# Kernel optimization log

Hardware: AMD Instinct MI355X
Metric: run time of the kernel (lower is better)

The kernel has to match this reference:

```python
import math
import jax, jax.numpy as jnp
import numpy as np

E = 1024
H = 16
HD = E // H
MLP = 4 * E
EPS = 1e-6


def setup_inputs() -> dict:
    key = jax.random.key(0)
    ks = jax.random.split(key, 12)
    s = lambda fan_in: 1.0 / math.sqrt(fan_in)
    return {
        "x": jax.random.normal(ks[0], (8, 1024, E), dtype=jnp.float32),
        "ln1_g": jnp.ones((E,), jnp.float32),
        "ln1_b": jnp.zeros((E,), jnp.float32),
        "w_qkv": jax.random.normal(ks[1], (E, 3 * E), jnp.float32) * s(E),
        "b_qkv": jnp.zeros((3 * E,), jnp.float32),
        "w_o": jax.random.normal(ks[2], (E, E), jnp.float32) * s(E),
        "b_o": jnp.zeros((E,), jnp.float32),
        "ln2_g": jnp.ones((E,), jnp.float32),
        "ln2_b": jnp.zeros((E,), jnp.float32),
        "w_fc1": jax.random.normal(ks[3], (E, MLP), jnp.float32) * s(E),
        "b_fc1": jnp.zeros((MLP,), jnp.float32),
        "w_fc2": jax.random.normal(ks[4], (MLP, E), jnp.float32) * s(MLP),
        "b_fc2": jnp.zeros((E,), jnp.float32),
    }


def _layernorm(x, g, b):
    mu = jnp.mean(x, axis=-1, keepdims=True)
    var = jnp.mean(jnp.square(x - mu), axis=-1, keepdims=True)
    return (x - mu) * jax.lax.rsqrt(var + EPS) * g + b


def _attn(x, w_qkv, b_qkv, w_o, b_o):
    B, N, _ = x.shape
    qkv = (x @ w_qkv + b_qkv).reshape(B, N, 3, H, HD)
    q, k, v = qkv[:, :, 0], qkv[:, :, 1], qkv[:, :, 2]  # [B,N,H,HD]
    scores = jnp.einsum("bnhd,bmhd->bhnm", q, k) / math.sqrt(HD)
    probs = jax.nn.softmax(scores, axis=-1)
    out = jnp.einsum("bhnm,bmhd->bnhd", probs, v).reshape(B, N, H * HD)
    return out @ w_o + b_o


def reference(x, ln1_g, ln1_b, w_qkv, b_qkv, w_o, b_o, ln2_g, ln2_b,
              w_fc1, b_fc1, w_fc2, b_fc2):
    # pre-LN attention block with residual
    x = x + _attn(_layernorm(x, ln1_g, ln1_b), w_qkv, b_qkv, w_o, b_o)
    # pre-LN MLP block with residual (exact GELU, matching torch nn.GELU)
    h = _layernorm(x, ln2_g, ln2_b) @ w_fc1 + b_fc1
    h = jax.nn.gelu(h, approximate=False)
    x = x + (h @ w_fc2 + b_fc2)
    return x
```

## Files before the change

kernel.cpp:

```cpp
#include <hip/hip_runtime.h>
#include <stdint.h>

typedef unsigned short u16;
typedef __bf16 bf16x8 __attribute__((ext_vector_type(8)));
typedef float f32x4 __attribute__((ext_vector_type(4)));

#define GLD16(gp, lp) __builtin_amdgcn_global_load_lds( \
    (__attribute__((address_space(1))) void*)(uintptr_t)(gp), \
    (__attribute__((address_space(3))) void*)(uintptr_t)(lp), 16, 0, 0)

__device__ __forceinline__ u16 f2bf(float f) {
  uint32_t u = __builtin_bit_cast(uint32_t, f);
  u += 0x7FFFu + ((u >> 16) & 1u);
  return (u16)(u >> 16);
}

__global__ __launch_bounds__(256) void wtrans(const float* __restrict__ w,
                                              u16* __restrict__ wt, int K, int Nn) {
  __shared__ float tile[64][68];
  const int c0 = blockIdx.x << 6, r0 = blockIdx.y << 6;
  const int t = threadIdx.x, tr = t >> 2, tc = t & 3;
#pragma unroll
  for (int p = 0; p < 4; ++p) {
    float4 v = *(const float4*)&w[(size_t)(r0 + tr) * Nn + c0 + tc * 4 + p * 16];
    tile[tr][tc * 4 + p * 16 + 0] = v.x;
    tile[tr][tc * 4 + p * 16 + 1] = v.y;
    tile[tr][tc * 4 + p * 16 + 2] = v.z;
    tile[tr][tc * 4 + p * 16 + 3] = v.w;
  }
  __syncthreads();
#pragma unroll
  for (int p = 0; p < 4; ++p) {
    u16 e0 = f2bf(tile[tc * 4 + p * 16 + 0][tr]);
    u16 e1 = f2bf(tile[tc * 4 + p * 16 + 1][tr]);
    u16 e2 = f2bf(tile[tc * 4 + p * 16 + 2][tr]);
    u16 e3 = f2bf(tile[tc * 4 + p * 16 + 3][tr]);
    uint2 o;
    o.x = (uint32_t)e0 | ((uint32_t)e1 << 16);
    o.y = (uint32_t)e2 | ((uint32_t)e3 << 16);
    *(uint2*)&wt[(size_t)(c0 + tr) * K + r0 + tc * 4 + p * 16] = o;
  }
}

__global__ __launch_bounds__(256) void lnorm(const float* x, const float* __restrict__ g,
                                             const float* __restrict__ bta,
                                             u16* __restrict__ out) {
  const int lane = threadIdx.x & 63, wid = threadIdx.x >> 6;
  const size_t token = (size_t)blockIdx.x * 4 + wid;
  const float* row = x + token * 1024;
  float v[16];
#pragma unroll
  for (int i = 0; i < 4; ++i) {
    float4 f = *(const float4*)&row[(lane + i * 64) * 4];
    v[i * 4 + 0] = f.x; v[i * 4 + 1] = f.y; v[i * 4 + 2] = f.z; v[i * 4 + 3] = f.w;
  }
  float s = 0.f, s2 = 0.f;
#pragma unroll
  for (int i = 0; i < 16; ++i) { s += v[i]; s2 += v[i] * v[i]; }
  for (int off = 1; off < 64; off <<= 1) {
    s += __shfl_xor(s, off);
    s2 += __shfl_xor(s2, off);
  }
  const float mu = s * (1.0f / 1024.0f);
  const float var = s2 * (1.0f / 1024.0f) - mu * mu;
  const float rstd = rsqrtf(var + 1e-6f);
  u16* orow = out + token * 1024;
#pragma unroll
  for (int i = 0; i < 4; ++i) {
    const int c = (lane + i * 64) * 4;
    float4 gv = *(const float4*)&g[c];
    float4 bv = *(const float4*)&bta[c];
    u16 e0 = f2bf((v[i * 4 + 0] - mu) * rstd * gv.x + bv.x);
    u16 e1 = f2bf((v[i * 4 + 1] - mu) * rstd * gv.y + bv.y);
    u16 e2 = f2bf((v[i * 4 + 2] - mu) * rstd * gv.z + bv.z);
    u16 e3 = f2bf((v[i * 4 + 3] - mu) * rstd * gv.w + bv.w);
    uint2 o;
    o.x = (uint32_t)e0 | ((uint32_t)e1 << 16);
    o.y = (uint32_t)e2 | ((uint32_t)e3 << 16);
    *(uint2*)&orow[c] = o;
  }
}

template <int EPI>
__global__ __launch_bounds__(256) void gemm128(const u16* __restrict__ A,
                                               const u16* __restrict__ Bt,
                                               const float* __restrict__ bias,
                                               const float* res, void* Cout,
                                               int Ndim, int K, float qscale, int qlimit) {
  __shared__ __align__(16) u16 ldsA[2][4096];
  __shared__ __align__(16) u16 ldsB[2][4096];
  const int tid = threadIdx.x;
  const int lane = tid & 63;
  const int wid = tid >> 6;
  const int wm = wid & 1, wn = wid >> 1;
  const int m0 = blockIdx.y << 7, n0 = blockIdx.x << 7;

  const int srow = lane >> 2;
  const int slc = (lane & 3) ^ ((srow ^ (srow >> 2)) & 3);
  const u16* Ag = A + (size_t)(m0 + 32 * wid + srow) * K + slc * 8;
  const u16* Bg = Bt + (size_t)(n0 + 32 * wid + srow) * K + slc * 8;
  const size_t rstep = (size_t)16 * K;

  const int rrow = lane & 15;
  const int rc = ((lane >> 4) ^ ((rrow ^ (rrow >> 2)) & 3)) * 16;

  const f32x4 fzero = {0.f, 0.f, 0.f, 0.f};
  f32x4 acc[4][4];
#pragma unroll
  for (int i = 0; i < 4; ++i)
#pragma unroll
    for (int j = 0; j < 4; ++j) acc[i][j] = fzero;

  const int nk = K >> 5;
  GLD16(Ag, &ldsA[0][(2 * wid + 0) * 512]);
  GLD16(Ag + rstep, &ldsA[0][(2 * wid + 1) * 512]);
  GLD16(Bg, &ldsB[0][(2 * wid + 0) * 512]);
  GLD16(Bg + rstep, &ldsB[0][(2 * wid + 1) * 512]);
  __syncthreads();
  for (int kt = 0; kt < nk; ++kt) {
    const int cur = kt & 1;
    if (kt + 1 < nk) {
      const u16* a = Ag + (size_t)(kt + 1) * 32;
      const u16* b = Bg + (size_t)(kt + 1) * 32;
      GLD16(a, &ldsA[cur ^ 1][(2 * wid + 0) * 512]);
      GLD16(a + rstep, &ldsA[cur ^ 1][(2 * wid + 1) * 512]);
      GLD16(b, &ldsB[cur ^ 1][(2 * wid + 0) * 512]);
      GLD16(b + rstep, &ldsB[cur ^ 1][(2 * wid + 1) * 512]);
    }
    bf16x8 af[4], bfr[4];
#pragma unroll
    for (int mf = 0; mf < 4; ++mf)
      af[mf] = *(const bf16x8*)((const char*)&ldsA[cur][0] +
                                (wm * 64 + mf * 16 + rrow) * 64 + rc);
#pragma unroll
    for (int nf = 0; nf < 4; ++nf)
      bfr[nf] = *(const bf16x8*)((const char*)&ldsB[cur][0] +
                                 (wn * 64 + nf * 16 + rrow) * 64 + rc);
#pragma unroll
    for (int mf = 0; mf < 4; ++mf)
#pragma unroll
      for (int nf = 0; nf < 4; ++nf)
        acc[mf][nf] =
            __builtin_amdgcn_mfma_f32_16x16x32_bf16(af[mf], bfr[nf], acc[mf][nf], 0, 0, 0);
    __syncthreads();
  }
  const int g4 = (lane >> 4) << 2;
  const float cs = (EPI == 0 && n0 < qlimit) ? qscale : 1.0f;
#pragma unroll
  for (int nf = 0; nf < 4; ++nf) {
    const int col = n0 + wn * 64 + nf * 16 + rrow;
    const float bv = bias[col];
#pragma unroll
    for (int mf = 0; mf < 4; ++mf) {
#pragma unroll
      for (int r = 0; r < 4; ++r) {
        const int row = m0 + wm * 64 + mf * 16 + g4 + r;
        float v = acc[mf][nf][r] + bv;
        if (EPI == 0) v *= cs;
        if (EPI == 1) v = 0.5f * v * (1.0f + erff(v * 0.70710678118654752f));
        if (EPI == 2) {
          v += res[(size_t)row * Ndim + col];
          ((float*)Cout)[(size_t)row * Ndim + col] = v;
        } else {
          ((u16*)Cout)[(size_t)row * Ndim + col] = f2bf(v);
        }
      }
    }
  }
}

__global__ __launch_bounds__(256) void vtrans(const u16* __restrict__ qkv,
                                              u16* __restrict__ vt) {
  const int bh = blockIdx.y, b = bh >> 4, h = bh & 15;
  const int n0 = blockIdx.x << 6;
  __shared__ __align__(16) u16 tile[64][72];
  const int t = threadIdx.x, r = t >> 2, c = t & 3;
  const u16* src = qkv + (size_t)((b << 10) + n0 + r) * 3072 + 2048 + (h << 6);
#pragma unroll
  for (int p = 0; p < 2; ++p)
    *(uint4*)&tile[r][(c * 2 + p) * 8] = *(const uint4*)(src + (c * 2 + p) * 8);
  __syncthreads();
  u16* dst = vt + (size_t)((bh << 6) + r) * 1024 + n0;
#pragma unroll
  for (int p = 0; p < 2; ++p) {
    u16 o[8];
#pragma unroll
    for (int j = 0; j < 8; ++j) o[j] = tile[(c * 2 + p) * 8 + j][r];
    uint4 w;
    w.x = (uint32_t)o[0] | ((uint32_t)o[1] << 16);
    w.y = (uint32_t)o[2] | ((uint32_t)o[3] << 16);
    w.z = (uint32_t)o[4] | ((uint32_t)o[5] << 16);
    w.w = (uint32_t)o[6] | ((uint32_t)o[7] << 16);
    *(uint4*)&dst[(c * 2 + p) * 8] = w;
  }
}

__global__ __launch_bounds__(256) void attn64(const u16* __restrict__ qkv,
                                              const u16* __restrict__ vt,
                                              u16* __restrict__ aout) {
  const int bh = blockIdx.y, b = bh >> 4, h = bh & 15;
  const int q0 = blockIdx.x << 6;
  const int tid = threadIdx.x, lane = tid & 63, wid = tid >> 6;
  __shared__ __align__(16) u16 kl[4096];
  __shared__ __align__(16) u16 vl[4096];
  __shared__ __align__(16) u16 pl[4][1152];

  const int rrow = lane & 15;
  const int g = lane >> 4;
  const u16* qrow = qkv + (size_t)((b << 10) + q0 + (wid << 4) + rrow) * 3072 + (h << 6);
  bf16x8 qf0 = *(const bf16x8*)(qrow + (g << 3));
  bf16x8 qf1 = *(const bf16x8*)(qrow + 32 + (g << 3));

  const int sr = lane >> 3;
  const int lc = (lane & 7) ^ sr;
  const u16* kbase = qkv + (size_t)(b << 10) * 3072 + 1024 + (h << 6) +
                     (size_t)(16 * wid + sr) * 3072 + lc * 8;
  const u16* vbase = vt + (size_t)(bh << 6) * 1024 + (size_t)(16 * wid + sr) * 1024 + lc * 8;

  const f32x4 fzero = {0.f, 0.f, 0.f, 0.f};
  f32x4 oacc[4];
#pragma unroll
  for (int i = 0; i < 4; ++i) oacc[i] = fzero;
  f32x4 lacc = fzero;
  const int rcb = lane & 7;
  u16* plw = &pl[wid][0];

  for (int t = 0; t < 16; ++t) {
    const int kt0 = t << 6;
    GLD16(kbase + (size_t)kt0 * 3072, &kl[(2 * wid + 0) * 512]);
    GLD16(kbase + (size_t)kt0 * 3072 + 8 * 3072, &kl[(2 * wid + 1) * 512]);
    GLD16(vbase + kt0, &vl[(2 * wid + 0) * 512]);
    GLD16(vbase + kt0 + 8 * 1024, &vl[(2 * wid + 1) * 512]);
    __syncthreads();

    f32x4 s4[4];
#pragma unroll
    for (int i = 0; i < 4; ++i) s4[i] = fzero;
#pragma unroll
    for (int nf = 0; nf < 4; ++nf) {
      bf16x8 k0 = *(const bf16x8*)((const char*)kl + (nf * 16 + rrow) * 128 +
                                   ((g + 0) ^ rcb) * 16);
      bf16x8 k1 = *(const bf16x8*)((const char*)kl + (nf * 16 + rrow) * 128 +
                                   ((g + 4) ^ rcb) * 16);
      s4[nf] = __builtin_amdgcn_mfma_f32_16x16x32_bf16(k0, qf0, s4[nf], 0, 0, 0);
      s4[nf] = __builtin_amdgcn_mfma_f32_16x16x32_bf16(k1, qf1, s4[nf], 0, 0, 0);
    }

#pragma unroll
    for (int nf = 0; nf < 4; ++nf) {
      float p0 = exp2f(s4[nf][0]);
      float p1 = exp2f(s4[nf][1]);
      float p2 = exp2f(s4[nf][2]);
      float p3 = exp2f(s4[nf][3]);
      f32x4 pv = {p0, p1, p2, p3};
      lacc += pv;
      uint32_t a0 = __builtin_bit_cast(uint32_t, p0) + 0x8000u;
      uint32_t a1 = __builtin_bit_cast(uint32_t, p1) + 0x8000u;
      uint32_t a2 = __builtin_bit_cast(uint32_t, p2) + 0x8000u;
      uint32_t a3 = __builtin_bit_cast(uint32_t, p3) + 0x8000u;
      uint2 w;
      w.x = __builtin_amdgcn_perm(a1, a0, 0x07060302);
      w.y = __builtin_amdgcn_perm(a3, a2, 0x07060302);
      *(uint2*)(plw + rrow * 72 + nf * 16 + (g << 2)) = w;
    }

    bf16x8 pf0 = *(const bf16x8*)((const char*)plw + rrow * 144 + (g << 4));
    bf16x8 pf1 = *(const bf16x8*)((const char*)plw + rrow * 144 + (g << 4) + 64);
#pragma unroll
    for (int nf = 0; nf < 4; ++nf) {
      bf16x8 v0 = *(const bf16x8*)((const char*)vl + (nf * 16 + rrow) * 128 +
                                   ((g + 0) ^ rcb) * 16);
      bf16x8 v1 = *(const bf16x8*)((const char*)vl + (nf * 16 + rrow) * 128 +
                                   ((g + 4) ^ rcb) * 16);
      oacc[nf] = __builtin_amdgcn_mfma_f32_16x16x32_bf16(pf0, v0, oacc[nf], 0, 0, 0);
      oacc[nf] = __builtin_amdgcn_mfma_f32_16x16x32_bf16(pf1, v1, oacc[nf], 0, 0, 0);
    }
    __syncthreads();
  }

  float lsum = lacc[0] + lacc[1] + lacc[2] + lacc[3];
  lsum += __shfl_xor(lsum, 16);
  lsum += __shfl_xor(lsum, 32);
  const float inv = 1.0f / lsum;
  float invq[4];
#pragma unroll
  for (int r = 0; r < 4; ++r) {
    int bi = __builtin_amdgcn_ds_bpermute(((g << 2) + r) << 2,
                                          __builtin_bit_cast(int, inv));
    invq[r] = __builtin_bit_cast(float, bi);
  }
  u16* ob = aout + (size_t)((b << 10) + q0 + (wid << 4)) * 1024 + (h << 6);
#pragma unroll
  for (int nf = 0; nf < 4; ++nf)
#pragma unroll
    for (int r = 0; r < 4; ++r)
      ob[(size_t)(g * 4 + r) * 1024 + nf * 16 + rrow] = f2bf(oacc[nf][r] * invq[r]);
}

extern "C" void kernel_launch(void* const* d_in, const int* in_sizes, int n_in,
                              void* d_out, int out_size, void* d_ws, size_t ws_size,
                              hipStream_t stream) {
  const float* x = (const float*)d_in[0];
  const float* ln1_g = (const float*)d_in[1];
  const float* ln1_b = (const float*)d_in[2];
  const float* w_qkv = (const float*)d_in[3];
  const float* b_qkv = (const float*)d_in[4];
  const float* w_o = (const float*)d_in[5];
  const float* b_o = (const float*)d_in[6];
  const float* ln2_g = (const float*)d_in[7];
  const float* ln2_b = (const float*)d_in[8];
  const float* w_fc1 = (const float*)d_in[9];
  const float* b_fc1 = (const float*)d_in[10];
  const float* w_fc2 = (const float*)d_in[11];
  const float* b_fc2 = (const float*)d_in[12];
  float* out = (float*)d_out;

  char* w = (char*)d_ws;
  u16* wqkvT = (u16*)w; w += (size_t)3072 * 1024 * 2;
  u16* woT   = (u16*)w; w += (size_t)1024 * 1024 * 2;
  u16* wfc1T = (u16*)w; w += (size_t)4096 * 1024 * 2;
  u16* wfc2T = (u16*)w; w += (size_t)1024 * 4096 * 2;
  u16* xn    = (u16*)w; w += (size_t)8192 * 1024 * 2;
  u16* qkvb  = (u16*)w; w += (size_t)8192 * 3072 * 2;
  u16* vtb   = (u16*)w; w += (size_t)128 * 64 * 1024 * 2;
  u16* attnb = (u16*)w; w += (size_t)8192 * 1024 * 2;
  u16* hbuf  = qkvb;

  const float QS = 0.18033688011112042f;

  wtrans<<<dim3(48, 16), 256, 0, stream>>>(w_qkv, wqkvT, 1024, 3072);
  wtrans<<<dim3(16, 16), 256, 0, stream>>>(w_o, woT, 1024, 1024);
  wtrans<<<dim3(64, 16), 256, 0, stream>>>(w_fc1, wfc1T, 1024, 4096);
  wtrans<<<dim3(16, 64), 256, 0, stream>>>(w_fc2, wfc2T, 4096, 1024);

  lnorm<<<2048, 256, 0, stream>>>(x, ln1_g, ln1_b, xn);
  gemm128<0><<<dim3(24, 64), 256, 0, stream>>>(xn, wqkvT, b_qkv, nullptr, qkvb, 3072, 1024, QS, 1024);
  vtrans<<<dim3(16, 128), 256, 0, stream>>>(qkvb, vtb);
  attn64<<<dim3(16, 128), 256, 0, stream>>>(qkvb, vtb, attnb);
  gemm128<2><<<dim3(8, 64), 256, 0, stream>>>(attnb, woT, b_o, x, out, 1024, 1024, 1.f, 0);
  lnorm<<<2048, 256, 0, stream>>>(out, ln2_g, ln2_b, xn);
  gemm128<1><<<dim3(32, 64), 256, 0, stream>>>(xn, wfc1T, b_fc1, nullptr, hbuf, 4096, 1024, 1.f, 0);
  gemm128<2><<<dim3(8, 64), 256, 0, stream>>>(hbuf, wfc2T, b_fc2, out, out, 1024, 4096, 1.f, 0);
}
```

Baseline: 434.9 us.

## Replace 128x128 GEMM with 256-row tiles, triple-buffered pipeline and XCD swizzle

Replaces the 128x128 four-wave GEMM with an eight-wave kernel using 256xBN tiles (BN 256 for the QKV/FC1 GEMMs, 128 for the output projections). It adds a three-stage LDS pipeline with explicit vmcnt waits and a single barrier per k-step, and interleaves prefetch issues with MFMA groups under s_setprio. Block indices are remapped so consecutive blocks on the same XCD share M rows. The goal is more data reuse per tile, fewer barriers and better L2 locality, at the cost of more LDS and registers per block and fewer blocks in the grid.

Result: faster. 418.8 us (-3.7%).

```diff
diff --git a/kernel.cpp b/kernel.cpp
--- a/kernel.cpp
+++ b/kernel.cpp
@@ -8,6 +8,9 @@
 #define GLD16(gp, lp) __builtin_amdgcn_global_load_lds( \
     (__attribute__((address_space(1))) void*)(uintptr_t)(gp), \
     (__attribute__((address_space(3))) void*)(uintptr_t)(lp), 16, 0, 0)
+
+#define WAITVM(N) asm volatile("s_waitcnt vmcnt(" #N ")" ::: "memory")
+#define BARRIER() asm volatile("s_barrier" ::: "memory")
 
 __device__ __forceinline__ u16 f2bf(float f) {
   uint32_t u = __builtin_bit_cast(uint32_t, f);
@@ -81,82 +84,141 @@
   }
 }
 
-template <int EPI>
-__global__ __launch_bounds__(256) void gemm128(const u16* __restrict__ A,
-                                               const u16* __restrict__ Bt,
-                                               const float* __restrict__ bias,
-                                               const float* res, void* Cout,
-                                               int Ndim, int K, float qscale, int qlimit) {
-  __shared__ __align__(16) u16 ldsA[2][4096];
-  __shared__ __align__(16) u16 ldsB[2][4096];
-  const int tid = threadIdx.x;
-  const int lane = tid & 63;
-  const int wid = tid >> 6;
-  const int wm = wid & 1, wn = wid >> 1;
-  const int m0 = blockIdx.y << 7, n0 = blockIdx.x << 7;
-
-  const int srow = lane >> 2;
-  const int slc = (lane & 3) ^ ((srow ^ (srow >> 2)) & 3);
-  const u16* Ag = A + (size_t)(m0 + 32 * wid + srow) * K + slc * 8;
-  const u16* Bg = Bt + (size_t)(n0 + 32 * wid + srow) * K + slc * 8;
-  const size_t rstep = (size_t)16 * K;
+template <int EPI, int BN>
+__global__ __launch_bounds__(512, 2) void gemm256(const u16* __restrict__ A,
+                                                  const u16* __restrict__ Bt,
+                                                  const float* __restrict__ bias,
+                                                  const float* res, void* Cout,
+                                                  int Ndim, int K, float qscale,
+                                                  int qlimit, int gn) {
+  constexpr int MF = (BN == 256) ? 8 : 4;
+  constexpr int HMF = MF / 2;
+  constexpr int WMS = (BN == 256) ? 128 : 64;
+  constexpr int SLOT = 8192 + BN * 32;
+  __shared__ __align__(16) u16 lds[3][SLOT];
+
+  const int tid = threadIdx.x, lane = tid & 63, wid = tid >> 6;
+  const int wm = (BN == 256) ? (wid >> 2) : (wid >> 1);
+  const int wn = (BN == 256) ? (wid & 3) : (wid & 1);
+
+  const int wg = blockIdx.x;
+  const int swz = (wg & 7) * ((int)gridDim.x >> 3) + (wg >> 3);
+  const int mblk = swz / gn;
+  const int nb = swz - mblk * gn;
+  const int m0 = mblk << 8;
+  const int n0 = nb * BN;
+
+  const int srow = tid >> 2;
+  const int slc = (tid & 3) ^ ((srow ^ (srow >> 2)) & 3);
+  const u16* Ag = A + (size_t)(m0 + srow) * K + slc * 8;
+  const u16* Bg = Bt + (size_t)(n0 + srow) * K + slc * 8;
+  const size_t rstep = (size_t)128 * K;
 
   const int rrow = lane & 15;
   const int rc = ((lane >> 4) ^ ((rrow ^ (rrow >> 2)) & 3)) * 16;
+  const int aRow0 = wm * WMS + rrow;
+  const int bRow0 = wn * 64 + rrow;
 
   const f32x4 fzero = {0.f, 0.f, 0.f, 0.f};
-  f32x4 acc[4][4];
-#pragma unroll
-  for (int i = 0; i < 4; ++i)
+  f32x4 acc[MF][4];
+#pragma unroll
+  for (int i = 0; i < MF; ++i)
 #pragma unroll
     for (int j = 0; j < 4; ++j) acc[i][j] = fzero;
 
   const int nk = K >> 5;
-  GLD16(Ag, &ldsA[0][(2 * wid + 0) * 512]);
-  GLD16(Ag + rstep, &ldsA[0][(2 * wid + 1) * 512]);
-  GLD16(Bg, &ldsB[0][(2 * wid + 0) * 512]);
-  GLD16(Bg + rstep, &ldsB[0][(2 * wid + 1) * 512]);
-  __syncthreads();
+
+#define SA0(kt, s) GLD16(Ag + (size_t)(kt) * 32, &lds[s][wid * 512])
+#define SA1(kt, s) GLD16(Ag + rstep + (size_t)(kt) * 32, &lds[s][4096 + wid * 512])
+#define SB0(kt, s) GLD16(Bg + (size_t)(kt) * 32, &lds[s][8192 + wid * 512])
+#define SB1(kt, s) GLD16(Bg + rstep + (size_t)(kt) * 32, &lds[s][12288 + wid * 512])
+
+  SA0(0, 0); SA1(0, 0); SB0(0, 0);
+  if constexpr (BN == 256) SB1(0, 0);
+  SA0(1, 1); SA1(1, 1); SB0(1, 1);
+  if constexpr (BN == 256) SB1(1, 1);
+
+  int cs = 0, ss = 2;
   for (int kt = 0; kt < nk; ++kt) {
-    const int cur = kt & 1;
     if (kt + 1 < nk) {
-      const u16* a = Ag + (size_t)(kt + 1) * 32;
-      const u16* b = Bg + (size_t)(kt + 1) * 32;
-      GLD16(a, &ldsA[cur ^ 1][(2 * wid + 0) * 512]);
-      GLD16(a + rstep, &ldsA[cur ^ 1][(2 * wid + 1) * 512]);
-      GLD16(b, &ldsB[cur ^ 1][(2 * wid + 0) * 512]);
-      GLD16(b + rstep, &ldsB[cur ^ 1][(2 * wid + 1) * 512]);
-    }
-    bf16x8 af[4], bfr[4];
-#pragma unroll
-    for (int mf = 0; mf < 4; ++mf)
-      af[mf] = *(const bf16x8*)((const char*)&ldsA[cur][0] +
-                                (wm * 64 + mf * 16 + rrow) * 64 + rc);
-#pragma unroll
-    for (int nf = 0; nf < 4; ++nf)
-      bfr[nf] = *(const bf16x8*)((const char*)&ldsB[cur][0] +
-                                 (wn * 64 + nf * 16 + rrow) * 64 + rc);
-#pragma unroll
-    for (int mf = 0; mf < 4; ++mf)
-#pragma unroll
-      for (int nf = 0; nf < 4; ++nf)
-        acc[mf][nf] =
-            __builtin_amdgcn_mfma_f32_16x16x32_bf16(af[mf], bfr[nf], acc[mf][nf], 0, 0, 0);
-    __syncthreads();
-  }
+      if constexpr (BN == 256) WAITVM(4); else WAITVM(3);
+    } else {
+      WAITVM(0);
+    }
+    BARRIER();
+    const bool pf = (kt + 2 < nk);
+    const char* la = (const char*)&lds[cs][0];
+    const char* lb = la + 16384;
+    bf16x8 af[MF], bv[4];
+    if (pf) SA0(kt + 2, ss);
+#pragma unroll
+    for (int i = 0; i < HMF; ++i)
+      af[i] = *(const bf16x8*)(la + (aRow0 + i * 16) * 64 + rc);
+    bv[0] = *(const bf16x8*)(lb + (bRow0 + 0) * 64 + rc);
+    bv[1] = *(const bf16x8*)(lb + (bRow0 + 16) * 64 + rc);
+    __builtin_amdgcn_s_setprio(1);
+#pragma unroll
+    for (int i = 0; i < HMF; ++i)
+#pragma unroll
+      for (int j = 0; j < 2; ++j)
+        acc[i][j] = __builtin_amdgcn_mfma_f32_16x16x32_bf16(af[i], bv[j], acc[i][j], 0, 0, 0);
+    __builtin_amdgcn_s_setprio(0);
+    if (pf) SA1(kt + 2, ss);
+#pragma unroll
+    for (int i = 0; i < HMF; ++i)
+      af[HMF + i] = *(const bf16x8*)(la + (aRow0 + (HMF + i) * 16) * 64 + rc);
+    __builtin_amdgcn_s_setprio(1);
+#pragma unroll
+    for (int i = 0; i < HMF; ++i)
+#pragma unroll
+      for (int j = 0; j < 2; ++j)
+        acc[HMF + i][j] =
+            __builtin_amdgcn_mfma_f32_16x16x32_bf16(af[HMF + i], bv[j], acc[HMF + i][j], 0, 0, 0);
+    __builtin_amdgcn_s_setprio(0);
+    if (pf) SB0(kt + 2, ss);
+    bv[2] = *(const bf16x8*)(lb + (bRow0 + 32) * 64 + rc);
+    bv[3] = *(const bf16x8*)(lb + (bRow0 + 48) * 64 + rc);
+    __builtin_amdgcn_s_setprio(1);
+#pragma unroll
+    for (int i = 0; i < HMF; ++i)
+#pragma unroll
+      for (int j = 0; j < 2; ++j)
+        acc[HMF + i][2 + j] =
+            __builtin_amdgcn_mfma_f32_16x16x32_bf16(af[HMF + i], bv[2 + j], acc[HMF + i][2 + j], 0, 0, 0);
+    __builtin_amdgcn_s_setprio(0);
+    if constexpr (BN == 256) {
+      if (pf) SB1(kt + 2, ss);
+    }
+    __builtin_amdgcn_s_setprio(1);
+#pragma unroll
+    for (int i = 0; i < HMF; ++i)
+#pragma unroll
+      for (int j = 0; j < 2; ++j)
+        acc[i][2 + j] =
+            __builtin_amdgcn_mfma_f32_16x16x32_bf16(af[i], bv[2 + j], acc[i][2 + j], 0, 0, 0);
+    __builtin_amdgcn_s_setprio(0);
+
+    cs = (cs == 2) ? 0 : cs + 1;
+    ss = (ss == 2) ? 0 : ss + 1;
+  }
+#undef SA0
+#undef SA1
+#undef SB0
+#undef SB1
+
   const int g4 = (lane >> 4) << 2;
-  const float cs = (EPI == 0 && n0 < qlimit) ? qscale : 1.0f;
 #pragma unroll
   for (int nf = 0; nf < 4; ++nf) {
     const int col = n0 + wn * 64 + nf * 16 + rrow;
-    const float bv = bias[col];
-#pragma unroll
-    for (int mf = 0; mf < 4; ++mf) {
+    const float bvb = bias[col];
+    const float csf = (EPI == 0 && col < qlimit) ? qscale : 1.0f;
+#pragma unroll
+    for (int mf = 0; mf < MF; ++mf) {
 #pragma unroll
       for (int r = 0; r < 4; ++r) {
-        const int row = m0 + wm * 64 + mf * 16 + g4 + r;
-        float v = acc[mf][nf][r] + bv;
-        if (EPI == 0) v *= cs;
+        const int row = m0 + wm * WMS + mf * 16 + g4 + r;
+        float v = acc[mf][nf][r] + bvb;
+        if (EPI == 0) v *= csf;
         if (EPI == 1) v = 0.5f * v * (1.0f + erff(v * 0.70710678118654752f));
         if (EPI == 2) {
           v += res[(size_t)row * Ndim + col];
@@ -334,11 +396,11 @@
   wtrans<<<dim3(16, 64), 256, 0, stream>>>(w_fc2, wfc2T, 4096, 1024);
 
   lnorm<<<2048, 256, 0, stream>>>(x, ln1_g, ln1_b, xn);
-  gemm128<0><<<dim3(24, 64), 256, 0, stream>>>(xn, wqkvT, b_qkv, nullptr, qkvb, 3072, 1024, QS, 1024);
+  gemm256<0, 256><<<384, 512, 0, stream>>>(xn, wqkvT, b_qkv, nullptr, qkvb, 3072, 1024, QS, 1024, 12);
   vtrans<<<dim3(16, 128), 256, 0, stream>>>(qkvb, vtb);
   attn64<<<dim3(16, 128), 256, 0, stream>>>(qkvb, vtb, attnb);
-  gemm128<2><<<dim3(8, 64), 256, 0, stream>>>(attnb, woT, b_o, x, out, 1024, 1024, 1.f, 0);
+  gemm256<2, 128><<<256, 512, 0, stream>>>(attnb, woT, b_o, x, out, 1024, 1024, 1.f, 0, 8);
   lnorm<<<2048, 256, 0, stream>>>(out, ln2_g, ln2_b, xn);
-  gemm128<1><<<dim3(32, 64), 256, 0, stream>>>(xn, wfc1T, b_fc1, nullptr, hbuf, 4096, 1024, 1.f, 0);
-  gemm128<2><<<dim3(8, 64), 256, 0, stream>>>(hbuf, wfc2T, b_fc2, out, out, 1024, 4096, 1.f, 0);
-}
+  gemm256<1, 256><<<512, 512, 0, stream>>>(xn, wfc1T, b_fc1, nullptr, hbuf, 4096, 1024, 1.f, 0, 16);
+  gemm256<2, 128><<<256, 512, 0, stream>>>(hbuf, wfc2T, b_fc2, out, out, 1024, 4096, 1.f, 0, 8);
+}
```

## Replace GEMM with 256x128 tile, 4-stage LDS pipeline and XCD-aware block swizzle

Applied to the files above, without the earlier changes.

Rewrites the bf16 MFMA GEMM to use 512-thread blocks computing 256x128 tiles. Global-to-LDS loads now run through a 4-stage ring with explicit vmcnt waits and raw barriers, and MFMA issue priority is raised around the compute phases. A 1D grid is remapped with a swizzle so neighbouring tiles land on the same XCD for L2 reuse. The goal is to hide global memory latency and raise MFMA utilisation, at the cost of 96KB of LDS per block and fragile hand-managed wait counts.

Result: faster. 416.3 us (-4.3%).

```diff
diff --git a/kernel.cpp b/kernel.cpp
--- a/kernel.cpp
+++ b/kernel.cpp
@@ -8,6 +8,10 @@
 #define GLD16(gp, lp) __builtin_amdgcn_global_load_lds( \
     (__attribute__((address_space(1))) void*)(uintptr_t)(gp), \
     (__attribute__((address_space(3))) void*)(uintptr_t)(lp), 16, 0, 0)
+
+#define WAITVM(N) asm volatile("s_waitcnt vmcnt(" #N ")" ::: "memory")
+#define BARRIER() asm volatile("s_barrier" ::: "memory")
+#define MM(a, b, c) __builtin_amdgcn_mfma_f32_16x16x32_bf16(a, b, c, 0, 0, 0)
 
 __device__ __forceinline__ u16 f2bf(float f) {
   uint32_t u = __builtin_bit_cast(uint32_t, f);
@@ -82,27 +86,39 @@
 }
 
 template <int EPI>
-__global__ __launch_bounds__(256) void gemm128(const u16* __restrict__ A,
-                                               const u16* __restrict__ Bt,
-                                               const float* __restrict__ bias,
-                                               const float* res, void* Cout,
-                                               int Ndim, int K, float qscale, int qlimit) {
-  __shared__ __align__(16) u16 ldsA[2][4096];
-  __shared__ __align__(16) u16 ldsB[2][4096];
-  const int tid = threadIdx.x;
-  const int lane = tid & 63;
-  const int wid = tid >> 6;
-  const int wm = wid & 1, wn = wid >> 1;
-  const int m0 = blockIdx.y << 7, n0 = blockIdx.x << 7;
-
-  const int srow = lane >> 2;
-  const int slc = (lane & 3) ^ ((srow ^ (srow >> 2)) & 3);
-  const u16* Ag = A + (size_t)(m0 + 32 * wid + srow) * K + slc * 8;
-  const u16* Bg = Bt + (size_t)(n0 + 32 * wid + srow) * K + slc * 8;
-  const size_t rstep = (size_t)16 * K;
-
-  const int rrow = lane & 15;
-  const int rc = ((lane >> 4) ^ ((rrow ^ (rrow >> 2)) & 3)) * 16;
+__global__ __launch_bounds__(512, 2) void gemmp(const u16* __restrict__ A,
+                                                const u16* __restrict__ Bt,
+                                                const float* __restrict__ bias,
+                                                const float* res, void* Cout,
+                                                int Ndim, int K, float qscale,
+                                                int qlimit, int gn) {
+  __shared__ __align__(16) u16 lds[4][12288];
+  const int tid = threadIdx.x, lane = tid & 63, wid = tid >> 6;
+  const int wm = wid >> 1, wn = wid & 1;
+
+  const int wg = blockIdx.x;
+  const int swz = (wg & 7) * ((int)gridDim.x >> 3) + (wg >> 3);
+  const int mblk = swz / gn, nb = swz - mblk * gn;
+  const int m0 = mblk << 8, n0 = nb << 7;
+
+  const int srow = tid >> 2;
+  const int sc = (tid & 3) ^ ((tid >> 3) & 3);
+  const u16* Ag0 = A + (size_t)(m0 + srow) * K + sc * 8;
+  const u16* Ag1 = Ag0 + (size_t)128 * K;
+  const u16* Bg = Bt + (size_t)(n0 + srow) * K + sc * 8;
+
+  u16* lb = &lds[0][0];
+  const int rrow = lane & 15, g = lane >> 4;
+  const int xg = g ^ ((rrow >> 1) & 3);
+  const int aoff = (wm * 64 + rrow) * 64 + xg * 16;
+  const int boff = 16384 + (wn * 64 + rrow) * 64 + xg * 16;
+  const char* pA[4];
+  const char* pB[4];
+#pragma unroll
+  for (int s = 0; s < 4; ++s) {
+    pA[s] = (const char*)lb + s * 24576 + aoff;
+    pB[s] = (const char*)lb + s * 24576 + boff;
+  }
 
   const f32x4 fzero = {0.f, 0.f, 0.f, 0.f};
   f32x4 acc[4][4];
@@ -111,52 +127,81 @@
 #pragma unroll
     for (int j = 0; j < 4; ++j) acc[i][j] = fzero;
 
-  const int nk = K >> 5;
-  GLD16(Ag, &ldsA[0][(2 * wid + 0) * 512]);
-  GLD16(Ag + rstep, &ldsA[0][(2 * wid + 1) * 512]);
-  GLD16(Bg, &ldsB[0][(2 * wid + 0) * 512]);
-  GLD16(Bg + rstep, &ldsB[0][(2 * wid + 1) * 512]);
-  __syncthreads();
-  for (int kt = 0; kt < nk; ++kt) {
-    const int cur = kt & 1;
-    if (kt + 1 < nk) {
-      const u16* a = Ag + (size_t)(kt + 1) * 32;
-      const u16* b = Bg + (size_t)(kt + 1) * 32;
-      GLD16(a, &ldsA[cur ^ 1][(2 * wid + 0) * 512]);
-      GLD16(a + rstep, &ldsA[cur ^ 1][(2 * wid + 1) * 512]);
-      GLD16(b, &ldsB[cur ^ 1][(2 * wid + 0) * 512]);
-      GLD16(b + rstep, &ldsB[cur ^ 1][(2 * wid + 1) * 512]);
-    }
-    bf16x8 af[4], bfr[4];
-#pragma unroll
-    for (int mf = 0; mf < 4; ++mf)
-      af[mf] = *(const bf16x8*)((const char*)&ldsA[cur][0] +
-                                (wm * 64 + mf * 16 + rrow) * 64 + rc);
-#pragma unroll
-    for (int nf = 0; nf < 4; ++nf)
-      bfr[nf] = *(const bf16x8*)((const char*)&ldsB[cur][0] +
-                                 (wn * 64 + nf * 16 + rrow) * 64 + rc);
-#pragma unroll
-    for (int mf = 0; mf < 4; ++mf)
-#pragma unroll
-      for (int nf = 0; nf < 4; ++nf)
-        acc[mf][nf] =
-            __builtin_amdgcn_mfma_f32_16x16x32_bf16(af[mf], bfr[nf], acc[mf][nf], 0, 0, 0);
-    __syncthreads();
-  }
+#define STG(tt, ss) do { \
+    GLD16(Ag0 + (tt) * 32, lb + (ss) * 12288 + wid * 512); \
+    GLD16(Ag1 + (tt) * 32, lb + (ss) * 12288 + 4096 + wid * 512); \
+    GLD16(Bg + (tt) * 32, lb + (ss) * 12288 + 8192 + wid * 512); \
+  } while (0)
+
+#define PH(dt, DOSTG, WVA) do { \
+    bf16x8 af0 = *(const bf16x8*)(pA[(dt)] + 0); \
+    bf16x8 af1 = *(const bf16x8*)(pA[(dt)] + 1024); \
+    bf16x8 af2 = *(const bf16x8*)(pA[(dt)] + 2048); \
+    bf16x8 af3 = *(const bf16x8*)(pA[(dt)] + 3072); \
+    bf16x8 bf0 = *(const bf16x8*)(pB[(dt)] + 0); \
+    bf16x8 bf1 = *(const bf16x8*)(pB[(dt)] + 1024); \
+    bf16x8 bf2 = *(const bf16x8*)(pB[(dt)] + 2048); \
+    bf16x8 bf3 = *(const bf16x8*)(pB[(dt)] + 3072); \
+    if (DOSTG) STG((dt) + 3, ((dt) + 3) & 3); \
+    WVA; \
+    BARRIER(); \
+    __builtin_amdgcn_s_setprio(1); \
+    acc[0][0] = MM(af0, bf0, acc[0][0]); \
+    acc[1][0] = MM(af1, bf0, acc[1][0]); \
+    acc[2][0] = MM(af2, bf0, acc[2][0]); \
+    acc[3][0] = MM(af3, bf0, acc[3][0]); \
+    acc[0][1] = MM(af0, bf1, acc[0][1]); \
+    acc[1][1] = MM(af1, bf1, acc[1][1]); \
+    acc[2][1] = MM(af2, bf1, acc[2][1]); \
+    acc[3][1] = MM(af3, bf1, acc[3][1]); \
+    acc[0][2] = MM(af0, bf2, acc[0][2]); \
+    acc[1][2] = MM(af1, bf2, acc[1][2]); \
+    acc[2][2] = MM(af2, bf2, acc[2][2]); \
+    acc[3][2] = MM(af3, bf2, acc[3][2]); \
+    acc[0][3] = MM(af0, bf3, acc[0][3]); \
+    acc[1][3] = MM(af1, bf3, acc[1][3]); \
+    acc[2][3] = MM(af2, bf3, acc[2][3]); \
+    acc[3][3] = MM(af3, bf3, acc[3][3]); \
+    __builtin_amdgcn_s_setprio(0); \
+    BARRIER(); \
+  } while (0)
+
+  const int nT = K >> 5;
+  STG(0, 0);
+  STG(1, 1);
+  STG(2, 2);
+  WAITVM(6);
+  BARRIER();
+  const int nG = nT >> 2;
+  for (int gi = 0; gi < nG - 1; ++gi) {
+    PH(0, true, WAITVM(6));
+    PH(1, true, WAITVM(6));
+    PH(2, true, WAITVM(6));
+    PH(3, true, WAITVM(6));
+    Ag0 += 128;
+    Ag1 += 128;
+    Bg += 128;
+  }
+  PH(0, true, WAITVM(6));
+  PH(1, false, WAITVM(3));
+  PH(2, false, WAITVM(0));
+  PH(3, false, (void)0);
+#undef PH
+#undef STG
+
   const int g4 = (lane >> 4) << 2;
-  const float cs = (EPI == 0 && n0 < qlimit) ? qscale : 1.0f;
 #pragma unroll
   for (int nf = 0; nf < 4; ++nf) {
     const int col = n0 + wn * 64 + nf * 16 + rrow;
-    const float bv = bias[col];
+    const float bvb = bias[col];
+    const float csf = (EPI == 0 && col < qlimit) ? qscale : 1.0f;
 #pragma unroll
     for (int mf = 0; mf < 4; ++mf) {
 #pragma unroll
       for (int r = 0; r < 4; ++r) {
         const int row = m0 + wm * 64 + mf * 16 + g4 + r;
-        float v = acc[mf][nf][r] + bv;
-        if (EPI == 0) v *= cs;
+        float v = acc[mf][nf][r] + bvb;
+        if (EPI == 0) v *= csf;
         if (EPI == 1) v = 0.5f * v * (1.0f + erff(v * 0.70710678118654752f));
         if (EPI == 2) {
           v += res[(size_t)row * Ndim + col];
@@ -334,11 +379,11 @@
   wtrans<<<dim3(16, 64), 256, 0, stream>>>(w_fc2, wfc2T, 4096, 1024);
 
   lnorm<<<2048, 256, 0, stream>>>(x, ln1_g, ln1_b, xn);
-  gemm128<0><<<dim3(24, 64), 256, 0, stream>>>(xn, wqkvT, b_qkv, nullptr, qkvb, 3072, 1024, QS, 1024);
+  gemmp<0><<<768, 512, 0, stream>>>(xn, wqkvT, b_qkv, nullptr, qkvb, 3072, 1024, QS, 1024, 24);
   vtrans<<<dim3(16, 128), 256, 0, stream>>>(qkvb, vtb);
   attn64<<<dim3(16, 128), 256, 0, stream>>>(qkvb, vtb, attnb);
-  gemm128<2><<<dim3(8, 64), 256, 0, stream>>>(attnb, woT, b_o, x, out, 1024, 1024, 1.f, 0);
+  gemmp<2><<<256, 512, 0, stream>>>(attnb, woT, b_o, x, out, 1024, 1024, 1.f, 0, 8);
   lnorm<<<2048, 256, 0, stream>>>(out, ln2_g, ln2_b, xn);
-  gemm128<1><<<dim3(32, 64), 256, 0, stream>>>(xn, wfc1T, b_fc1, nullptr, hbuf, 4096, 1024, 1.f, 0);
-  gemm128<2><<<dim3(8, 64), 256, 0, stream>>>(hbuf, wfc2T, b_fc2, out, out, 1024, 4096, 1.f, 0);
-}
+  gemmp<1><<<1024, 512, 0, stream>>>(xn, wfc1T, b_fc1, nullptr, hbuf, 4096, 1024, 1.f, 0, 32);
+  gemmp<2><<<256, 512, 0, stream>>>(hbuf, wfc2T, b_fc2, out, out, 1024, 4096, 1.f, 0, 8);
+}
```

## Replace 128x128 GEMM with 256x256 tiles, 4-stage pipeline, split-K atomics

Applied to the files above, without the earlier changes.

Replaces the 128x128 double-buffered GEMM with a 512-thread 256x256 tile kernel. It uses a 4-slot LDS ring with two tiles in flight, explicit vmcnt waits and raw barriers, MFMA priority raising, and a grouped workgroup swizzle for L2 reuse. The residual GEMMs (w_o, fc2) now use split-K=2 with atomicAdd into an output that a device memcpy of x pre-initialises. The aim is more data reuse per tile, deeper latency hiding and better occupancy of the small-N GEMMs. The cost is larger register and LDS pressure, atomic traffic, nondeterministic summation order and an extra 32MB copy.

Result: slower. 480.5 us (+10.5%).

```diff
diff --git a/kernel.cpp b/kernel.cpp
--- a/kernel.cpp
+++ b/kernel.cpp
@@ -8,6 +8,10 @@
 #define GLD16(gp, lp) __builtin_amdgcn_global_load_lds( \
     (__attribute__((address_space(1))) void*)(uintptr_t)(gp), \
     (__attribute__((address_space(3))) void*)(uintptr_t)(lp), 16, 0, 0)
+
+#define WAITVM(N) asm volatile("s_waitcnt vmcnt(" #N ")" ::: "memory")
+#define BARRIER() asm volatile("s_barrier" ::: "memory")
+#define MM(a, b, c) __builtin_amdgcn_mfma_f32_16x16x32_bf16(a, b, c, 0, 0, 0)
 
 __device__ __forceinline__ u16 f2bf(float f) {
   uint32_t u = __builtin_bit_cast(uint32_t, f);
@@ -82,85 +86,92 @@
 }
 
 template <int EPI>
-__global__ __launch_bounds__(256) void gemm128(const u16* __restrict__ A,
-                                               const u16* __restrict__ Bt,
-                                               const float* __restrict__ bias,
-                                               const float* res, void* Cout,
-                                               int Ndim, int K, float qscale, int qlimit) {
-  __shared__ __align__(16) u16 ldsA[2][4096];
-  __shared__ __align__(16) u16 ldsB[2][4096];
-  const int tid = threadIdx.x;
-  const int lane = tid & 63;
-  const int wid = tid >> 6;
-  const int wm = wid & 1, wn = wid >> 1;
-  const int m0 = blockIdx.y << 7, n0 = blockIdx.x << 7;
-
-  const int srow = lane >> 2;
-  const int slc = (lane & 3) ^ ((srow ^ (srow >> 2)) & 3);
-  const u16* Ag = A + (size_t)(m0 + 32 * wid + srow) * K + slc * 8;
-  const u16* Bg = Bt + (size_t)(n0 + 32 * wid + srow) * K + slc * 8;
-  const size_t rstep = (size_t)16 * K;
-
-  const int rrow = lane & 15;
-  const int rc = ((lane >> 4) ^ ((rrow ^ (rrow >> 2)) & 3)) * 16;
+__global__ __launch_bounds__(512, 2) void gemmk(const u16* __restrict__ A,
+                                                const u16* __restrict__ Bt,
+                                                const float* __restrict__ bias,
+                                                void* Cout, int Ndim, int K, int nT,
+                                                float qscale, int qlimit, int gn) {
+  __shared__ __align__(16) u16 lds[4][16384];
+  const int tid = threadIdx.x, lane = tid & 63, wid = tid >> 6;
+  const int wm = wid >> 2, wn = wid & 3;
+
+  const int wg = blockIdx.x;
+  const int swz = (wg & 7) * ((int)gridDim.x >> 3) + (wg >> 3);
+  const int mblk = swz / gn, nb = swz - mblk * gn;
+  const int m0 = mblk << 8, n0 = nb << 8;
+  const int koff = blockIdx.y * (nT << 5);
+
+  const int srow = tid >> 2;
+  const int gsub = (tid & 3) ^ ((tid >> 3) & 3);
+  const u16* Ag = A + koff + (size_t)(m0 + srow) * K + gsub * 8;
+  const u16* Bg = Bt + koff + (size_t)(n0 + srow) * K + gsub * 8;
+  const size_t rstep = (size_t)128 * K;
+  char* lb = (char*)&lds[0][0];
+
+  const int rrow = lane & 15, g = lane >> 4;
+  const int xg = g ^ ((rrow >> 1) & 3);
+  const int aoff = (wm * 128 + rrow) * 64 + xg * 16;
+  const int boff = 16384 + (wn * 64 + rrow) * 64 + xg * 16;
 
   const f32x4 fzero = {0.f, 0.f, 0.f, 0.f};
-  f32x4 acc[4][4];
-#pragma unroll
-  for (int i = 0; i < 4; ++i)
+  f32x4 acc[8][4];
+#pragma unroll
+  for (int i = 0; i < 8; ++i)
 #pragma unroll
     for (int j = 0; j < 4; ++j) acc[i][j] = fzero;
 
-  const int nk = K >> 5;
-  GLD16(Ag, &ldsA[0][(2 * wid + 0) * 512]);
-  GLD16(Ag + rstep, &ldsA[0][(2 * wid + 1) * 512]);
-  GLD16(Bg, &ldsB[0][(2 * wid + 0) * 512]);
-  GLD16(Bg + rstep, &ldsB[0][(2 * wid + 1) * 512]);
-  __syncthreads();
-  for (int kt = 0; kt < nk; ++kt) {
-    const int cur = kt & 1;
-    if (kt + 1 < nk) {
-      const u16* a = Ag + (size_t)(kt + 1) * 32;
-      const u16* b = Bg + (size_t)(kt + 1) * 32;
-      GLD16(a, &ldsA[cur ^ 1][(2 * wid + 0) * 512]);
-      GLD16(a + rstep, &ldsA[cur ^ 1][(2 * wid + 1) * 512]);
-      GLD16(b, &ldsB[cur ^ 1][(2 * wid + 0) * 512]);
-      GLD16(b + rstep, &ldsB[cur ^ 1][(2 * wid + 1) * 512]);
-    }
-    bf16x8 af[4], bfr[4];
-#pragma unroll
-    for (int mf = 0; mf < 4; ++mf)
-      af[mf] = *(const bf16x8*)((const char*)&ldsA[cur][0] +
-                                (wm * 64 + mf * 16 + rrow) * 64 + rc);
+#define STG(tt) do { \
+    char* d_ = lb + ((tt) & 3) * 32768; \
+    GLD16(Ag + (size_t)(tt) * 32, d_ + tid * 16); \
+    GLD16(Ag + rstep + (size_t)(tt) * 32, d_ + 8192 + tid * 16); \
+    GLD16(Bg + (size_t)(tt) * 32, d_ + 16384 + tid * 16); \
+    GLD16(Bg + rstep + (size_t)(tt) * 32, d_ + 24576 + tid * 16); \
+  } while (0)
+
+  STG(0);
+  STG(1);
+  WAITVM(4);
+  BARRIER();
+  for (int t = 0; t < nT; ++t) {
+    if (t + 2 < nT) STG(t + 2);
+    const char* sb = lb + (t & 3) * 32768;
+    bf16x8 bfr[4], af[8];
 #pragma unroll
     for (int nf = 0; nf < 4; ++nf)
-      bfr[nf] = *(const bf16x8*)((const char*)&ldsB[cur][0] +
-                                 (wn * 64 + nf * 16 + rrow) * 64 + rc);
-#pragma unroll
-    for (int mf = 0; mf < 4; ++mf)
+      bfr[nf] = *(const bf16x8*)(sb + boff + nf * 1024);
+#pragma unroll
+    for (int mf = 0; mf < 8; ++mf)
+      af[mf] = *(const bf16x8*)(sb + aoff + mf * 1024);
+    __builtin_amdgcn_s_setprio(1);
+#pragma unroll
+    for (int mf = 0; mf < 8; ++mf)
 #pragma unroll
       for (int nf = 0; nf < 4; ++nf)
-        acc[mf][nf] =
-            __builtin_amdgcn_mfma_f32_16x16x32_bf16(af[mf], bfr[nf], acc[mf][nf], 0, 0, 0);
-    __syncthreads();
-  }
+        acc[mf][nf] = MM(af[mf], bfr[nf], acc[mf][nf]);
+    __builtin_amdgcn_s_setprio(0);
+    if (t + 1 < nT) {
+      if (t < nT - 2) { WAITVM(4); } else { WAITVM(0); }
+      BARRIER();
+    }
+  }
+#undef STG
+
   const int g4 = (lane >> 4) << 2;
-  const float cs = (EPI == 0 && n0 < qlimit) ? qscale : 1.0f;
 #pragma unroll
   for (int nf = 0; nf < 4; ++nf) {
     const int col = n0 + wn * 64 + nf * 16 + rrow;
-    const float bv = bias[col];
-#pragma unroll
-    for (int mf = 0; mf < 4; ++mf) {
+    const float bvb = (EPI == 3 && blockIdx.y != 0) ? 0.0f : bias[col];
+    const float csf = (EPI == 0 && col < qlimit) ? qscale : 1.0f;
+#pragma unroll
+    for (int mf = 0; mf < 8; ++mf) {
 #pragma unroll
       for (int r = 0; r < 4; ++r) {
-        const int row = m0 + wm * 64 + mf * 16 + g4 + r;
-        float v = acc[mf][nf][r] + bv;
-        if (EPI == 0) v *= cs;
+        const int row = m0 + wm * 128 + mf * 16 + g4 + r;
+        float v = acc[mf][nf][r] + bvb;
+        if (EPI == 0) v *= csf;
         if (EPI == 1) v = 0.5f * v * (1.0f + erff(v * 0.70710678118654752f));
-        if (EPI == 2) {
-          v += res[(size_t)row * Ndim + col];
-          ((float*)Cout)[(size_t)row * Ndim + col] = v;
+        if (EPI == 3) {
+          atomicAdd((float*)Cout + (size_t)row * Ndim + col, v);
         } else {
           ((u16*)Cout)[(size_t)row * Ndim + col] = f2bf(v);
         }
@@ -334,11 +345,12 @@
   wtrans<<<dim3(16, 64), 256, 0, stream>>>(w_fc2, wfc2T, 4096, 1024);
 
   lnorm<<<2048, 256, 0, stream>>>(x, ln1_g, ln1_b, xn);
-  gemm128<0><<<dim3(24, 64), 256, 0, stream>>>(xn, wqkvT, b_qkv, nullptr, qkvb, 3072, 1024, QS, 1024);
+  gemmk<0><<<dim3(384, 1), 512, 0, stream>>>(xn, wqkvT, b_qkv, qkvb, 3072, 1024, 32, QS, 1024, 12);
   vtrans<<<dim3(16, 128), 256, 0, stream>>>(qkvb, vtb);
   attn64<<<dim3(16, 128), 256, 0, stream>>>(qkvb, vtb, attnb);
-  gemm128<2><<<dim3(8, 64), 256, 0, stream>>>(attnb, woT, b_o, x, out, 1024, 1024, 1.f, 0);
+  hipMemcpyAsync(out, x, (size_t)8192 * 1024 * 4, hipMemcpyDeviceToDevice, stream);
+  gemmk<3><<<dim3(128, 2), 512, 0, stream>>>(attnb, woT, b_o, out, 1024, 1024, 16, 1.f, 0, 4);
   lnorm<<<2048, 256, 0, stream>>>(out, ln2_g, ln2_b, xn);
-  gemm128<1><<<dim3(32, 64), 256, 0, stream>>>(xn, wfc1T, b_fc1, nullptr, hbuf, 4096, 1024, 1.f, 0);
-  gemm128<2><<<dim3(8, 64), 256, 0, stream>>>(hbuf, wfc2T, b_fc2, out, out, 1024, 4096, 1.f, 0);
-}
+  gemmk<1><<<dim3(512, 1), 512, 0, stream>>>(xn, wfc1T, b_fc1, hbuf, 4096, 1024, 32, 1.f, 0, 16);
+  gemmk<3><<<dim3(128, 2), 512, 0, stream>>>(hbuf, wfc2T, b_fc2, out, 1024, 4096, 64, 1.f, 0, 4);
+}
```
